# Performance work log

Hardware: AMD Instinct MI355X
Metric: run time of the kernel (lower is better)

## Reference

```python
import jax, jax.numpy as jnp
import numpy as np

N_ITERS = 3
EPS_ATTN = 1e-8
LN_EPS = 1e-5  # torch LayerNorm default

def _ln(x, w, b):
    mu = jnp.mean(x, axis=-1, keepdims=True)
    var = jnp.mean(jnp.square(x - mu), axis=-1, keepdims=True)
    return (x - mu) * jax.lax.rsqrt(var + LN_EPS) * w + b

def setup_inputs() -> dict:
    key = jax.random.key(0)
    ks = jax.random.split(key, 10)
    B, N, F, D, K = 64, 4096, 256, 128, 8
    return {
        "inputs": jax.random.normal(ks[0], (B, N, F), jnp.float32),
        "slot_init": jax.random.normal(ks[1], (1, K, D), jnp.float32) * 0.02,
        "Wq": jax.random.normal(ks[2], (D, D), jnp.float32) * (1.0 / np.sqrt(D)),
        "Wk": jax.random.normal(ks[3], (F, D), jnp.float32) * (1.0 / np.sqrt(F)),
        "Wv": jax.random.normal(ks[4], (F, D), jnp.float32) * (1.0 / np.sqrt(F)),
        "gru_wi": jax.random.normal(ks[5], (D, 3 * D), jnp.float32) * (1.0 / np.sqrt(D)),
        "gru_wh": jax.random.normal(ks[6], (D, 3 * D), jnp.float32) * (1.0 / np.sqrt(D)),
        "gru_bi": jnp.zeros((3 * D,), jnp.float32),
        "gru_bh": jnp.zeros((3 * D,), jnp.float32),
        "ln_in_w": jnp.ones((F,), jnp.float32),
        "ln_in_b": jnp.zeros((F,), jnp.float32),
        "ln_slots_w": jnp.ones((D,), jnp.float32),
        "ln_slots_b": jnp.zeros((D,), jnp.float32),
        "ln_mlp_w": jnp.ones((D,), jnp.float32),
        "ln_mlp_b": jnp.zeros((D,), jnp.float32),
        "mlp_w1": jax.random.normal(ks[7], (D, 2 * D), jnp.float32) * (1.0 / np.sqrt(D)),
        "mlp_b1": jnp.zeros((2 * D,), jnp.float32),
        "mlp_w2": jax.random.normal(ks[8], (2 * D, D), jnp.float32) * (1.0 / np.sqrt(2 * D)),
        "mlp_b2": jnp.zeros((D,), jnp.float32),
    }

def reference(inputs, slot_init, Wq, Wk, Wv, gru_wi, gru_wh, gru_bi, gru_bh,
              ln_in_w, ln_in_b, ln_slots_w, ln_slots_b, ln_mlp_w, ln_mlp_b,
              mlp_w1, mlp_b1, mlp_w2, mlp_b2):
    B, N, _ = inputs.shape
    D = Wq.shape[0]
    scale = jnp.asarray(D ** 0.5, inputs.dtype)
    x = _ln(inputs, ln_in_w, ln_in_b)
    k = x @ Wk            # [B, N, D]
    v = x @ Wv            # [B, N, D]
    slots = jnp.broadcast_to(slot_init, (B,) + slot_init.shape[1:])
    for _ in range(N_ITERS):
        slots_prev = slots
        q = _ln(slots, ln_slots_w, ln_slots_b) @ Wq         # [B, K, D]
        logits = jnp.einsum('bnd,bkd->bnk', k, q) / scale   # [B, N, K]
        attn = jax.nn.softmax(logits, axis=-1) + EPS_ATTN   # softmax over slots
        attn = attn / jnp.sum(attn, axis=1, keepdims=True)  # normalize over inputs
        updates = jnp.einsum('bnk,bnd->bkd', attn, v)       # [B, K, D]
        # GRUCell: x=updates, h=slots_prev (torch gate order: r, z, n)
        gx = updates @ gru_wi + gru_bi                      # [B, K, 3D]
        gh = slots_prev @ gru_wh + gru_bh
        r = jax.nn.sigmoid(gx[..., :D] + gh[..., :D])
        z = jax.nn.sigmoid(gx[..., D:2 * D] + gh[..., D:2 * D])
        n = jnp.tanh(gx[..., 2 * D:] + r * gh[..., 2 * D:])
        slots = (1.0 - z) * n + z * slots_prev
        h = jax.nn.relu(_ln(slots, ln_mlp_w, ln_mlp_b) @ mlp_w1 + mlp_b1)
        slots = slots + h @ mlp_w2 + mlp_b2
    return slots
```

## Files before the change

kernel.cpp:

```cpp
#include <hip/hip_runtime.h>
#include <math.h>

#define NB 64
#define NN 4096
#define NF 256
#define ND 128
#define NK 8
#define NCHUNK 16
#define CHROWS 256
#define MT 64

typedef unsigned int uint;
typedef unsigned short ushort;
typedef __attribute__((ext_vector_type(8))) short short8;
typedef __attribute__((ext_vector_type(4))) float floatx4;

constexpr float LN_EPS_C   = 1e-5f;
constexpr float EPS_ATTN_C = 1e-8f;
constexpr float INV_SCALE  = 0.08838834764831845f;

__device__ __forceinline__ float sigmoidf_(float x) { return 1.f / (1.f + expf(-x)); }
__device__ __forceinline__ ushort f2bf(float x) {
    uint u = __float_as_uint(x);
    return (ushort)((u + 0x7FFFu + ((u >> 16) & 1u)) >> 16);
}
__device__ __forceinline__ float bflo(uint u) { return __uint_as_float(u << 16); }
__device__ __forceinline__ float bfhi(uint u) { return __uint_as_float(u & 0xFFFF0000u); }

__global__ void init_slots_k(const float* __restrict__ init, float* __restrict__ slots) {
    int i = blockIdx.x * 256 + threadIdx.x;
    slots[i] = init[i & (NK * ND - 1)];
}

__global__ void wconv_k(const float* __restrict__ Wk, const float* __restrict__ Wv,
                        ushort* __restrict__ wt) {
    int c = blockIdx.x;
    int f = threadIdx.x;
    float v = (c < ND) ? Wk[(size_t)f * ND + c] : Wv[(size_t)f * ND + (c - ND)];
    wt[(size_t)c * NF + f] = f2bf(v);
}

__global__ __launch_bounds__(256) void ln_project_mfma(
    const float* __restrict__ inp, const ushort* __restrict__ wt,
    const float* __restrict__ lw, const float* __restrict__ lb,
    ushort* __restrict__ kout, ushort* __restrict__ vout) {
    __shared__ ushort As[MT][264];
    int t = threadIdx.x;
    size_t rowbase = (size_t)blockIdx.x * MT;

    {
        int rloc = t >> 4, seg = t & 15;
        const float4* lw4 = (const float4*)lw;
        const float4* lb4 = (const float4*)lb;
#pragma unroll
        for (int p = 0; p < 4; ++p) {
            int r = p * 16 + rloc;
            const float4* rowp = (const float4*)(inp + (rowbase + r) * NF);
            float4 xv[4];
            float sum = 0.f, sq = 0.f;
#pragma unroll
            for (int i = 0; i < 4; ++i) {
                xv[i] = rowp[seg * 4 + i];
                sum += xv[i].x + xv[i].y + xv[i].z + xv[i].w;
                sq += xv[i].x * xv[i].x + xv[i].y * xv[i].y + xv[i].z * xv[i].z + xv[i].w * xv[i].w;
            }
#pragma unroll
            for (int m = 8; m >= 1; m >>= 1) {
                sum += __shfl_xor(sum, m, 64);
                sq  += __shfl_xor(sq,  m, 64);
            }
            float mu = sum * (1.f / NF);
            float var = sq * (1.f / NF) - mu * mu;
            float rs = rsqrtf(var + LN_EPS_C);
#pragma unroll
            for (int i = 0; i < 4; ++i) {
                float4 w = lw4[seg * 4 + i], bb = lb4[seg * 4 + i], x = xv[i];
                float o0 = (x.x - mu) * rs * w.x + bb.x;
                float o1 = (x.y - mu) * rs * w.y + bb.y;
                float o2 = (x.z - mu) * rs * w.z + bb.z;
                float o3 = (x.w - mu) * rs * w.w + bb.w;
                uint2 pk;
                pk.x = (uint)f2bf(o0) | ((uint)f2bf(o1) << 16);
                pk.y = (uint)f2bf(o2) | ((uint)f2bf(o3) << 16);
                *(uint2*)&As[r][seg * 16 + i * 4] = pk;
            }
        }
    }
    __syncthreads();

    int w = t >> 6, lane = t & 63;
    int frow = lane & 15, q = lane >> 4;
    floatx4 acc[4][4];
#pragma unroll
    for (int mt = 0; mt < 4; ++mt)
#pragma unroll
        for (int nt = 0; nt < 4; ++nt) acc[mt][nt] = (floatx4)0.f;

#pragma unroll
    for (int ks = 0; ks < 8; ++ks) {
        short8 a[4], b[4];
#pragma unroll
        for (int mt = 0; mt < 4; ++mt)
            a[mt] = *(const short8*)&As[mt * 16 + frow][ks * 32 + q * 8];
#pragma unroll
        for (int nt = 0; nt < 4; ++nt) {
            int n = w * 64 + nt * 16 + frow;
            b[nt] = *(const short8*)(wt + (size_t)n * NF + ks * 32 + q * 8);
        }
#pragma unroll
        for (int mt = 0; mt < 4; ++mt)
#pragma unroll
            for (int nt = 0; nt < 4; ++nt)
                acc[mt][nt] = __builtin_amdgcn_mfma_f32_16x16x32_bf16(a[mt], b[nt], acc[mt][nt], 0, 0, 0);
    }

    ushort* outp = (w < 2) ? kout : vout;
    int cbase = (w & 1) * 64;
#pragma unroll
    for (int mt = 0; mt < 4; ++mt)
#pragma unroll
        for (int nt = 0; nt < 4; ++nt) {
            int c = cbase + nt * 16 + frow;
#pragma unroll
            for (int i = 0; i < 4; ++i) {
                int m = mt * 16 + q * 4 + i;
                outp[(rowbase + m) * ND + c] = f2bf(acc[mt][nt][i]);
            }
        }
}

__global__ __launch_bounds__(64) void q_kernel(
    const float* __restrict__ slots, const float* __restrict__ Wq,
    const float* __restrict__ lw, const float* __restrict__ lb,
    float* __restrict__ qout) {
    __shared__ float sln[ND];
    int bk = blockIdx.x;
    int t = threadIdx.x;
    const float* sp = slots + (size_t)bk * ND;
    float s0 = sp[t], s1 = sp[t + 64];
    float sum = s0 + s1, sq = s0 * s0 + s1 * s1;
#pragma unroll
    for (int m = 1; m < 64; m <<= 1) {
        sum += __shfl_xor(sum, m, 64);
        sq  += __shfl_xor(sq,  m, 64);
    }
    float mu = sum * (1.f / ND);
    float var = sq * (1.f / ND) - mu * mu;
    float rs = rsqrtf(var + LN_EPS_C);
    sln[t]      = (s0 - mu) * rs * lw[t]      + lb[t];
    sln[t + 64] = (s1 - mu) * rs * lw[t + 64] + lb[t + 64];
    __syncthreads();
    float q0 = 0.f, q1 = 0.f;
    for (int dd = 0; dd < ND; ++dd) {
        float v = sln[dd];
        q0 += v * Wq[dd * ND + t];
        q1 += v * Wq[dd * ND + 64 + t];
    }
    qout[(size_t)bk * ND + t] = q0;
    qout[(size_t)bk * ND + 64 + t] = q1;
}

__global__ __launch_bounds__(256) void attn_kernel(
    const ushort* __restrict__ kbuf, const ushort* __restrict__ vbuf,
    const float* __restrict__ qbuf, float* __restrict__ pU,
    float* __restrict__ pS) {
    __shared__ __align__(16) float attn_s[CHROWS * NK];
    __shared__ __align__(16) float qs[NK * ND];
    int t = threadIdx.x;
    int chunk = blockIdx.x, b = blockIdx.y;
    int n = chunk * CHROWS + t;

    ((float4*)qs)[t] = ((const float4*)(qbuf + (size_t)b * NK * ND))[t];
    __syncthreads();

    {
        const uint4* k16 = (const uint4*)(kbuf + ((size_t)b * NN + n) * ND);
        float lg[NK];
#pragma unroll
        for (int kk = 0; kk < NK; ++kk) lg[kk] = 0.f;
        for (int j = 0; j < 16; ++j) {
            uint4 kr = k16[j];
            float k0 = bflo(kr.x), k1 = bfhi(kr.x);
            float k2 = bflo(kr.y), k3 = bfhi(kr.y);
            float k4 = bflo(kr.z), k5 = bfhi(kr.z);
            float k6 = bflo(kr.w), k7 = bfhi(kr.w);
#pragma unroll
            for (int kk = 0; kk < NK; ++kk) {
                const float4* qp = (const float4*)(qs + kk * ND + j * 8);
                float4 q0 = qp[0], q1 = qp[1];
                lg[kk] += k0 * q0.x + k1 * q0.y + k2 * q0.z + k3 * q0.w
                        + k4 * q1.x + k5 * q1.y + k6 * q1.z + k7 * q1.w;
            }
        }
        float mx = -1e30f;
#pragma unroll
        for (int kk = 0; kk < NK; ++kk) { lg[kk] *= INV_SCALE; mx = fmaxf(mx, lg[kk]); }
        float se = 0.f;
        float e[NK];
#pragma unroll
        for (int kk = 0; kk < NK; ++kk) { e[kk] = expf(lg[kk] - mx); se += e[kk]; }
        float inv = 1.f / se;
#pragma unroll
        for (int kk = 0; kk < NK; ++kk) e[kk] = e[kk] * inv + EPS_ATTN_C;
        ((float4*)attn_s)[t * 2]     = make_float4(e[0], e[1], e[2], e[3]);
        ((float4*)attn_s)[t * 2 + 1] = make_float4(e[4], e[5], e[6], e[7]);
    }
    __syncthreads();

    {
        int dp = t & 63, kg = t >> 6;
        int d0 = dp * 2, kk0 = kg * 2;
        float4 ua = make_float4(0.f, 0.f, 0.f, 0.f);
        const uint* vp = (const uint*)(vbuf + ((size_t)b * NN + chunk * CHROWS) * ND + d0);
        for (int nn2 = 0; nn2 < CHROWS; ++nn2) {
            uint vr = vp[(size_t)nn2 * (ND / 2)];
            float v0 = bflo(vr), v1 = bfhi(vr);
            float2 a = *(const float2*)(attn_s + nn2 * NK + kk0);
            ua.x += a.x * v0; ua.y += a.x * v1;
            ua.z += a.y * v0; ua.w += a.y * v1;
        }
        size_t pb = ((size_t)chunk * NB + b) * (NK * ND);
        *(float2*)(pU + pb + (size_t)kk0 * ND + d0)       = make_float2(ua.x, ua.y);
        *(float2*)(pU + pb + (size_t)(kk0 + 1) * ND + d0) = make_float2(ua.z, ua.w);
    }
    __syncthreads();

    float4* as4 = (float4*)attn_s;
    for (int s2 = CHROWS / 2; s2 >= 1; s2 >>= 1) {
        if (t < s2) {
            float4 a0 = as4[t * 2],     b0 = as4[(t + s2) * 2];
            float4 a1 = as4[t * 2 + 1], b1 = as4[(t + s2) * 2 + 1];
            a0.x += b0.x; a0.y += b0.y; a0.z += b0.z; a0.w += b0.w;
            a1.x += b1.x; a1.y += b1.y; a1.z += b1.z; a1.w += b1.w;
            as4[t * 2] = a0; as4[t * 2 + 1] = a1;
        }
        __syncthreads();
    }
    if (t < NK) pS[((size_t)chunk * NB + b) * NK + t] = attn_s[t];
}

__global__ __launch_bounds__(128) void finish_kernel(
    const float* __restrict__ pU, const float* __restrict__ pS,
    const float* __restrict__ slots_in, const float* __restrict__ wi,
    const float* __restrict__ wh, const float* __restrict__ bi,
    const float* __restrict__ bh, const float* __restrict__ lnw,
    const float* __restrict__ lnb, const float* __restrict__ w1,
    const float* __restrict__ b1, const float* __restrict__ w2,
    const float* __restrict__ b2, float* __restrict__ slots_out,
    const float* __restrict__ Wq, const float* __restrict__ lqw,
    const float* __restrict__ lqb, float* __restrict__ qout, int compute_q) {
    __shared__ float updL[ND], spL[ND], lnL[ND], hL[2 * ND], lnQ[ND];
    __shared__ float red[2], red2[2], redq[2], redq2[2];
    int bk = blockIdx.x;
    int b = bk >> 3, kk = bk & 7;
    int d = threadIdx.x;

    float U = 0.f, S = 0.f;
    for (int c = 0; c < NCHUNK; ++c) {
        U += pU[((size_t)c * NB + b) * (NK * ND) + kk * ND + d];
        S += pS[((size_t)c * NB + b) * NK + kk];
    }
    float upd = U / S;
    float spd = slots_in[(size_t)bk * ND + d];
    updL[d] = upd;
    spL[d] = spd;
    __syncthreads();

    float gxr = bi[d], gxz = bi[ND + d], gxn = bi[2 * ND + d];
    float ghr = bh[d], ghz = bh[ND + d], ghn = bh[2 * ND + d];
    for (int dd = 0; dd < ND; ++dd) {
        float u = updL[dd], s = spL[dd];
        const float* wip = wi + (size_t)dd * 3 * ND;
        const float* whp = wh + (size_t)dd * 3 * ND;
        gxr += u * wip[d];          ghr += s * whp[d];
        gxz += u * wip[ND + d];     ghz += s * whp[ND + d];
        gxn += u * wip[2 * ND + d]; ghn += s * whp[2 * ND + d];
    }
    float r_ = sigmoidf_(gxr + ghr);
    float z_ = sigmoidf_(gxz + ghz);
    float nn_ = tanhf(gxn + r_ * ghn);
    float snew = (1.f - z_) * nn_ + z_ * spd;

    int wid = d >> 6;
    float sum = snew, sq = snew * snew;
#pragma unroll
    for (int m = 1; m < 64; m <<= 1) {
        sum += __shfl_xor(sum, m, 64);
        sq  += __shfl_xor(sq,  m, 64);
    }
    if ((d & 63) == 0) { red[wid] = sum; red2[wid] = sq; }
    __syncthreads();
    float tot = red[0] + red[1], totq = red2[0] + red2[1];
    float mu = tot * (1.f / ND);
    float var = totq * (1.f / ND) - mu * mu;
    float rs = rsqrtf(var + LN_EPS_C);
    lnL[d] = (snew - mu) * rs * lnw[d] + lnb[d];
    __syncthreads();

    float h0 = b1[d], h1 = b1[ND + d];
    for (int dd = 0; dd < ND; ++dd) {
        float lv = lnL[dd];
        h0 += lv * w1[(size_t)dd * 2 * ND + d];
        h1 += lv * w1[(size_t)dd * 2 * ND + ND + d];
    }
    hL[d] = fmaxf(h0, 0.f);
    hL[ND + d] = fmaxf(h1, 0.f);
    __syncthreads();
    float od = snew + b2[d];
    for (int j = 0; j < 2 * ND; ++j) od += hL[j] * w2[(size_t)j * ND + d];
    slots_out[(size_t)bk * ND + d] = od;

    if (compute_q) {
        float s2 = od, q2 = od * od;
#pragma unroll
        for (int m = 1; m < 64; m <<= 1) {
            s2 += __shfl_xor(s2, m, 64);
            q2 += __shfl_xor(q2, m, 64);
        }
        if ((d & 63) == 0) { redq[wid] = s2; redq2[wid] = q2; }
        __syncthreads();
        float tq = redq[0] + redq[1], tqq = redq2[0] + redq2[1];
        float muq = tq * (1.f / ND);
        float vq = tqq * (1.f / ND) - muq * muq;
        float rsq = rsqrtf(vq + LN_EPS_C);
        lnQ[d] = (od - muq) * rsq * lqw[d] + lqb[d];
        __syncthreads();
        float qc = 0.f;
        for (int dd = 0; dd < ND; ++dd) qc += lnQ[dd] * Wq[(size_t)dd * ND + d];
        qout[(size_t)bk * ND + d] = qc;
    }
}

extern "C" void kernel_launch(void* const* d_in, const int* in_sizes, int n_in,
                              void* d_out, int out_size, void* d_ws, size_t ws_size,
                              hipStream_t stream) {
    const float* inp       = (const float*)d_in[0];
    const float* slot_init = (const float*)d_in[1];
    const float* Wq        = (const float*)d_in[2];
    const float* Wk        = (const float*)d_in[3];
    const float* Wv        = (const float*)d_in[4];
    const float* gru_wi    = (const float*)d_in[5];
    const float* gru_wh    = (const float*)d_in[6];
    const float* gru_bi    = (const float*)d_in[7];
    const float* gru_bh    = (const float*)d_in[8];
    const float* ln_in_w   = (const float*)d_in[9];
    const float* ln_in_b   = (const float*)d_in[10];
    const float* ln_sl_w   = (const float*)d_in[11];
    const float* ln_sl_b   = (const float*)d_in[12];
    const float* ln_ml_w   = (const float*)d_in[13];
    const float* ln_ml_b   = (const float*)d_in[14];
    const float* mlp_w1    = (const float*)d_in[15];
    const float* mlp_b1    = (const float*)d_in[16];
    const float* mlp_w2    = (const float*)d_in[17];
    const float* mlp_b2    = (const float*)d_in[18];

    char* wsb = (char*)d_ws;
    ushort* kb = (ushort*)wsb;
    ushort* vb = kb + (size_t)NB * NN * ND;
    ushort* wt = vb + (size_t)NB * NN * ND;
    float* qb  = (float*)(wt + (size_t)NF * NF);
    float* sl  = qb + (size_t)NB * NK * ND;
    float* pU  = sl + (size_t)NB * NK * ND;
    float* pS  = pU + (size_t)NCHUNK * NB * NK * ND;

    init_slots_k<<<(NB * NK * ND) / 256, 256, 0, stream>>>(slot_init, sl);
    wconv_k<<<NF, NF, 0, stream>>>(Wk, Wv, wt);
    ln_project_mfma<<<(NB * NN) / MT, 256, 0, stream>>>(inp, wt, ln_in_w, ln_in_b, kb, vb);
    q_kernel<<<NB * NK, 64, 0, stream>>>(sl, Wq, ln_sl_w, ln_sl_b, qb);

    for (int it = 0; it < 3; ++it) {
        attn_kernel<<<dim3(NCHUNK, NB), 256, 0, stream>>>(kb, vb, qb, pU, pS);
        float* outp = (it == 2) ? (float*)d_out : sl;
        finish_kernel<<<NB * NK, 128, 0, stream>>>(pU, pS, sl, gru_wi, gru_wh,
                                                   gru_bi, gru_bh, ln_ml_w, ln_ml_b,
                                                   mlp_w1, mlp_b1, mlp_w2, mlp_b2, outp,
                                                   Wq, ln_sl_w, ln_sl_b, qb, (it < 2) ? 1 : 0);
    }
}
```

Measured before the change: 702.4 us.

## Store K transposed in dim-pair-major layout for coalesced attention loads

K is now written by the projection kernel in a [b][d/2][n] layout of packed bf16 pairs, so each attention thread reads one 32-bit word per dimension pair with consecutive threads reading consecutive addresses, instead of each thread streaming its own 256-byte row. The projection weights are pre-swizzled into MFMA fragment order so B-operand loads are contiguous per lane. V output is staged through shared memory to produce coalesced 16-byte row stores. This adds an extra sync and shuffle work in the projection epilogue and changes the q shared-memory layout to match the new K access pattern.

```diff
diff --git a/kernel.cpp b/kernel.cpp
--- a/kernel.cpp
+++ b/kernel.cpp
@@ -33,20 +33,30 @@
 }
 
 __global__ void wconv_k(const float* __restrict__ Wk, const float* __restrict__ Wv,
-                        ushort* __restrict__ wt) {
-    int c = blockIdx.x;
-    int f = threadIdx.x;
-    float v = (c < ND) ? Wk[(size_t)f * ND + c] : Wv[(size_t)f * ND + (c - ND)];
-    wt[(size_t)c * NF + f] = f2bf(v);
+                        ushort* __restrict__ wt2) {
+    int idx = blockIdx.x * 64 + threadIdx.x;
+    int c16 = idx >> 9, ks = (idx >> 6) & 7, lane = idx & 63;
+    int c = c16 * 16 + (lane & 15);
+    int f0 = ks * 32 + (lane >> 4) * 8;
+    ushort tmp[8];
+#pragma unroll
+    for (int j = 0; j < 8; ++j) {
+        int f = f0 + j;
+        float v = (c < ND) ? Wk[(size_t)f * ND + c] : Wv[(size_t)f * ND + (c - ND)];
+        tmp[j] = f2bf(v);
+    }
+    *(uint4*)(wt2 + (size_t)idx * 8) = *(uint4*)tmp;
 }
 
 __global__ __launch_bounds__(256) void ln_project_mfma(
-    const float* __restrict__ inp, const ushort* __restrict__ wt,
+    const float* __restrict__ inp, const ushort* __restrict__ wt2,
     const float* __restrict__ lw, const float* __restrict__ lb,
-    ushort* __restrict__ kout, ushort* __restrict__ vout) {
+    uint* __restrict__ kt2, ushort* __restrict__ vout) {
     __shared__ ushort As[MT][264];
     int t = threadIdx.x;
     size_t rowbase = (size_t)blockIdx.x * MT;
+    size_t bidx = rowbase >> 12;
+    size_t nbase = rowbase & (NN - 1);
 
     {
         int rloc = t >> 4, seg = t & 15;
@@ -100,33 +110,63 @@
     for (int ks = 0; ks < 8; ++ks) {
         short8 a[4], b[4];
 #pragma unroll
+        for (int nt = 0; nt < 4; ++nt)
+            b[nt] = *(const short8*)(wt2 + ((((size_t)(w * 4 + nt) * 8 + ks) * 64 + lane) * 8));
+#pragma unroll
         for (int mt = 0; mt < 4; ++mt)
             a[mt] = *(const short8*)&As[mt * 16 + frow][ks * 32 + q * 8];
 #pragma unroll
-        for (int nt = 0; nt < 4; ++nt) {
-            int n = w * 64 + nt * 16 + frow;
-            b[nt] = *(const short8*)(wt + (size_t)n * NF + ks * 32 + q * 8);
-        }
-#pragma unroll
         for (int mt = 0; mt < 4; ++mt)
 #pragma unroll
             for (int nt = 0; nt < 4; ++nt)
                 acc[mt][nt] = __builtin_amdgcn_mfma_f32_16x16x32_bf16(a[mt], b[nt], acc[mt][nt], 0, 0, 0);
     }
 
-    ushort* outp = (w < 2) ? kout : vout;
-    int cbase = (w & 1) * 64;
-#pragma unroll
-    for (int mt = 0; mt < 4; ++mt)
-#pragma unroll
-        for (int nt = 0; nt < 4; ++nt) {
-            int c = cbase + nt * 16 + frow;
-#pragma unroll
-            for (int i = 0; i < 4; ++i) {
-                int m = mt * 16 + q * 4 + i;
-                outp[(rowbase + m) * ND + c] = f2bf(acc[mt][nt][i]);
-            }
-        }
+    __syncthreads();
+
+    if (w < 2) {
+        int cbase = w * 64;
+#pragma unroll
+        for (int mt = 0; mt < 4; ++mt)
+#pragma unroll
+            for (int nt = 0; nt < 4; ++nt) {
+                int c = cbase + nt * 16 + frow;
+                uint u01 = (uint)f2bf(acc[mt][nt][0]) | ((uint)f2bf(acc[mt][nt][1]) << 16);
+                uint u23 = (uint)f2bf(acc[mt][nt][2]) | ((uint)f2bf(acc[mt][nt][3]) << 16);
+                uint p01 = __shfl_xor(u01, 1, 64);
+                uint p23 = __shfl_xor(u23, 1, 64);
+                if ((frow & 1) == 0) {
+                    uint4 out;
+                    out.x = (u01 & 0xFFFFu) | (p01 << 16);
+                    out.y = (u01 >> 16) | (p01 & 0xFFFF0000u);
+                    out.z = (u23 & 0xFFFFu) | (p23 << 16);
+                    out.w = (u23 >> 16) | (p23 & 0xFFFF0000u);
+                    size_t nloc = nbase + mt * 16 + q * 4;
+                    *(uint4*)(kt2 + (bidx * 64 + (size_t)(c >> 1)) * NN + nloc) = out;
+                }
+            }
+    } else {
+        int cbase = (w & 1) * 64;
+#pragma unroll
+        for (int mt = 0; mt < 4; ++mt)
+#pragma unroll
+            for (int nt = 0; nt < 4; ++nt) {
+                int c = cbase + nt * 16 + frow;
+#pragma unroll
+                for (int i = 0; i < 4; ++i)
+                    As[mt * 16 + q * 4 + i][c] = f2bf(acc[mt][nt][i]);
+            }
+    }
+    __syncthreads();
+
+    {
+        int r = t >> 2, part = t & 3;
+#pragma unroll
+        for (int u = 0; u < 4; ++u) {
+            uint4 val = *(const uint4*)&As[r][part * 32 + u * 8];
+            *(uint4*)(vout + (rowbase + r) * ND + part * 32 + u * 8) = val;
+        }
+    }
 }
 
 __global__ __launch_bounds__(64) void q_kernel(
@@ -161,35 +201,38 @@
 }
 
 __global__ __launch_bounds__(256) void attn_kernel(
-    const ushort* __restrict__ kbuf, const ushort* __restrict__ vbuf,
+    const uint* __restrict__ kt2, const ushort* __restrict__ vbuf,
     const float* __restrict__ qbuf, float* __restrict__ pU,
     float* __restrict__ pS) {
     __shared__ __align__(16) float attn_s[CHROWS * NK];
-    __shared__ __align__(16) float qs[NK * ND];
+    __shared__ __align__(16) float qs2[64 * 16];
     int t = threadIdx.x;
     int chunk = blockIdx.x, b = blockIdx.y;
     int n = chunk * CHROWS + t;
 
-    ((float4*)qs)[t] = ((const float4*)(qbuf + (size_t)b * NK * ND))[t];
+#pragma unroll
+    for (int p = 0; p < 4; ++p) {
+        int idx = p * 256 + t;
+        int kk = idx >> 7, d = idx & 127;
+        qs2[(d >> 1) * 16 + kk * 2 + (d & 1)] = qbuf[(size_t)b * NK * ND + idx];
+    }
     __syncthreads();
 
     {
-        const uint4* k16 = (const uint4*)(kbuf + ((size_t)b * NN + n) * ND);
+        const uint* ktp = kt2 + (size_t)b * 64 * NN + n;
         float lg[NK];
 #pragma unroll
         for (int kk = 0; kk < NK; ++kk) lg[kk] = 0.f;
-        for (int j = 0; j < 16; ++j) {
-            uint4 kr = k16[j];
-            float k0 = bflo(kr.x), k1 = bfhi(kr.x);
-            float k2 = bflo(kr.y), k3 = bfhi(kr.y);
-            float k4 = bflo(kr.z), k5 = bfhi(kr.z);
-            float k6 = bflo(kr.w), k7 = bfhi(kr.w);
-#pragma unroll
-            for (int kk = 0; kk < NK; ++kk) {
-                const float4* qp = (const float4*)(qs + kk * ND + j * 8);
-                float4 q0 = qp[0], q1 = qp[1];
-                lg[kk] += k0 * q0.x + k1 * q0.y + k2 * q0.z + k3 * q0.w
-                        + k4 * q1.x + k5 * q1.y + k6 * q1.z + k7 * q1.w;
+#pragma unroll 8
+        for (int j = 0; j < 64; ++j) {
+            uint kr = ktp[(size_t)j * NN];
+            float k0 = bflo(kr), k1 = bfhi(kr);
+            const float4* qp = (const float4*)(qs2 + j * 16);
+#pragma unroll
+            for (int c = 0; c < 4; ++c) {
+                float4 qq = qp[c];
+                lg[2 * c]     += k0 * qq.x + k1 * qq.y;
+                lg[2 * c + 1] += k0 * qq.z + k1 * qq.w;
             }
         }
         float mx = -1e30f;
@@ -355,21 +398,21 @@
     const float* mlp_b2    = (const float*)d_in[18];
 
     char* wsb = (char*)d_ws;
-    ushort* kb = (ushort*)wsb;
-    ushort* vb = kb + (size_t)NB * NN * ND;
-    ushort* wt = vb + (size_t)NB * NN * ND;
-    float* qb  = (float*)(wt + (size_t)NF * NF);
-    float* sl  = qb + (size_t)NB * NK * ND;
-    float* pU  = sl + (size_t)NB * NK * ND;
-    float* pS  = pU + (size_t)NCHUNK * NB * NK * ND;
+    uint* kt2   = (uint*)wsb;
+    ushort* vb  = (ushort*)(wsb + (size_t)NB * 64 * NN * 4);
+    ushort* wt2 = vb + (size_t)NB * NN * ND;
+    float* qb   = (float*)(wt2 + (size_t)NF * NF);
+    float* sl   = qb + (size_t)NB * NK * ND;
+    float* pU   = sl + (size_t)NB * NK * ND;
+    float* pS   = pU + (size_t)NCHUNK * NB * NK * ND;
 
     init_slots_k<<<(NB * NK * ND) / 256, 256, 0, stream>>>(slot_init, sl);
-    wconv_k<<<NF, NF, 0, stream>>>(Wk, Wv, wt);
-    ln_project_mfma<<<(NB * NN) / MT, 256, 0, stream>>>(inp, wt, ln_in_w, ln_in_b, kb, vb);
+    wconv_k<<<128, 64, 0, stream>>>(Wk, Wv, wt2);
+    ln_project_mfma<<<(NB * NN) / MT, 256, 0, stream>>>(inp, wt2, ln_in_w, ln_in_b, kt2, vb);
     q_kernel<<<NB * NK, 64, 0, stream>>>(sl, Wq, ln_sl_w, ln_sl_b, qb);
 
     for (int it = 0; it < 3; ++it) {
-        attn_kernel<<<dim3(NCHUNK, NB), 256, 0, stream>>>(kb, vb, qb, pU, pS);
+        attn_kernel<<<dim3(NCHUNK, NB), 256, 0, stream>>>(kt2, vb, qb, pU, pS);
         float* outp = (it == 2) ? (float*)d_out : sl;
         finish_kernel<<<NB * NK, 128, 0, stream>>>(pU, pS, sl, gru_wi, gru_wh,
                                                    gru_bi, gru_bh, ln_ml_w, ln_ml_b,
```

Result: no change. 690.8 us (-1.7%).
